# Optimization experiments

Measured on AMD Instinct MI355X. Metric: run time of the kernel, lower is better.

## Reference

```python
import jax, jax.numpy as jnp
import numpy as np

H = W = 224
N_LM = 8
BLOCK = 3  # patch is [x-3:x+3, y-3:y+3] -> 6x6


def _clip_coords(lm_float):
    # lm_float: [B, 16] normalized landmarks in [0,1]
    c = (lm_float * 224.0).astype(jnp.int32)
    c = jnp.where(c >= 219, 200, c)
    c = jnp.where(c <= 5, 8, c)
    return c.reshape(c.shape[0], N_LM, 2)


def _gather_patches(pred_map, coords):
    # pred_map: [B,1,H,W], coords: [B,8,2] int32 -> [B,8,36]
    B = pred_map.shape[0]
    x = coords[..., 0]  # [B,8]
    y = coords[..., 1]
    offs = jnp.arange(-BLOCK, BLOCK)  # 6 offsets
    xs = x[..., None] + offs          # [B,8,6]
    ys = y[..., None] + offs          # [B,8,6]
    b = jnp.arange(B)[:, None, None, None]
    # vectorized gather replacing the per-sample/per-landmark python loop
    patches = pred_map[b, 0, xs[:, :, :, None], ys[:, :, None, :]]  # [B,8,6,6]
    return patches.reshape(B, N_LM, (2 * BLOCK) ** 2)


def setup_inputs() -> dict:
    key = jax.random.key(0)
    ks = jax.random.split(key, 8)
    B = 512
    pred_map = jax.random.normal(ks[0], (B, 1, H, W), dtype=jnp.float32)
    Landmarks_GT = jax.random.uniform(ks[1], (B, 16), dtype=jnp.float32)
    d_in = H * W  # 50176
    s1 = 1.0 / np.sqrt(d_in)
    s2 = 1.0 / np.sqrt(512)
    s3 = 1.0 / np.sqrt(256)
    W1 = jax.random.uniform(ks[2], (d_in, 512), jnp.float32, -s1, s1)
    b1 = jax.random.uniform(ks[3], (512,), jnp.float32, -s1, s1)
    W2 = jax.random.uniform(ks[4], (512, 256), jnp.float32, -s2, s2)
    b2 = jax.random.uniform(ks[5], (256,), jnp.float32, -s2, s2)
    W3 = jax.random.uniform(ks[6], (256, 16), jnp.float32, -s3, s3)
    b3 = jax.random.uniform(ks[7], (16,), jnp.float32, -s3, s3)
    return {"pred_map": pred_map, "Landmarks_GT": Landmarks_GT,
            "W1": W1, "b1": b1, "W2": W2, "b2": b2, "W3": W3, "b3": b3}


def reference(pred_map, Landmarks_GT, W1, b1, W2, b2, W3, b3):
    B = pred_map.shape[0]
    # GT landmark patch gather
    gt_coords = _clip_coords(Landmarks_GT)
    GT_patch = _gather_patches(pred_map, gt_coords)  # [B,8,36]
    # MLP_Grah_Second on flattened pred_map
    flat = pred_map.reshape(B, -1)                   # [B,50176]
    h = jax.nn.relu(flat @ W1 + b1)
    h = jax.nn.relu(h @ W2 + b2)
    pred = jax.nn.sigmoid(h @ W3 + b3)               # [B,16]
    # predicted landmark patch gather
    pr_coords = _clip_coords(pred)
    Pred_patch = _gather_patches(pred_map, pr_coords)  # [B,8,36]
    return pred, GT_patch, Pred_patch
```

## Files before the change

kernel.cpp:

```cpp
#include <hip/hip_runtime.h>
#include <math.h>

typedef __fp16   h16x2 __attribute__((ext_vector_type(2)));
typedef _Float16 f16x8 __attribute__((ext_vector_type(8)));
typedef __attribute__((ext_vector_type(4))) float f32x4;

#define KDIM 50176
#define NDIM 512
#define MDIM 512
#define BM 256
#define BN 128
#define BK 32

__device__ __forceinline__ void split_pair(float a, float b, unsigned& hw, unsigned& lw) {
    h16x2 hp = __builtin_amdgcn_cvt_pkrtz(a, b);
    float ra = (a - (float)hp[0]) * 2048.0f;
    float rb = (b - (float)hp[1]) * 2048.0f;
    h16x2 lp = __builtin_amdgcn_cvt_pkrtz(ra, rb);
    union { h16x2 v; unsigned u; } cu;
    cu.v = hp; hw = cu.u;
    cu.v = lp; lw = cu.u;
}

__global__ __launch_bounds__(512, 2) void gemm1_mfma(
    const float* __restrict__ A,
    const float* __restrict__ W,
    float* __restrict__ part,
    int steps, int S)
{
    __shared__ unsigned short Ahs[2][256][40];
    __shared__ unsigned short Als[2][256][40];
    __shared__ unsigned short Bhs[2][128][40];
    __shared__ unsigned short Bls[2][128][40];

    const int t = threadIdx.x;

    const int nwg = 8 * S;
    int l = blockIdx.x;
    if ((nwg & 7) == 0) l = (l & 7) * (nwg >> 3) + (l >> 3);
    const int z = l >> 3, bm = l & 1, bn = (l >> 1) & 3;
    const int kbase = z * steps * BK;

    const int lane = t & 63, wave = t >> 6;
    const int wm = wave >> 1, wn2 = wave & 1;
    const int l15 = lane & 15, lh = lane >> 4;

    const bool isW = (t < 256);
    const int u = isW ? t : (t - 256);
    const int wkb = u & 7, wn0 = (u >> 3) * 4;
    const int achunk = u & 7, arow0 = u >> 3;

    f32x4 acc0[4][4], acc1[4][4];
#pragma unroll
    for (int i = 0; i < 4; ++i)
#pragma unroll
        for (int j = 0; j < 4; ++j) { acc0[i][j] = (f32x4)0.f; acc1[i][j] = (f32x4)0.f; }

    float4 reg[8];
    auto gload = [&](int s) {
        const int k0 = kbase + s * BK;
        if (isW) {
            const float* Wb = W + (size_t)k0 * NDIM + bn * BN + wn0;
#pragma unroll
            for (int i = 0; i < 4; ++i)
                reg[i] = *(const float4*)(Wb + (size_t)(wkb * 4 + i) * NDIM);
        } else {
            const float* Ab = A + (size_t)(bm * BM) * KDIM + k0 + achunk * 4;
#pragma unroll
            for (int j = 0; j < 8; ++j)
                reg[j] = *(const float4*)(Ab + (size_t)(arow0 + 32 * j) * KDIM);
        }
    };

    auto stageA = [&](int buf, int j) {
        unsigned h01, l01, h23, l23;
        split_pair(reg[j].x, reg[j].y, h01, l01);
        split_pair(reg[j].z, reg[j].w, h23, l23);
        *(uint2*)&Ahs[buf][arow0 + 32 * j][achunk * 4] = make_uint2(h01, h23);
        *(uint2*)&Als[buf][arow0 + 32 * j][achunk * 4] = make_uint2(l01, l23);
    };
    auto stageW = [&](int buf, int j) {
        unsigned h01, l01, h23, l23;
        split_pair(((const float*)&reg[0])[j] * 64.0f, ((const float*)&reg[1])[j] * 64.0f, h01, l01);
        split_pair(((const float*)&reg[2])[j] * 64.0f, ((const float*)&reg[3])[j] * 64.0f, h23, l23);
        *(uint2*)&Bhs[buf][wn0 + j][wkb * 4] = make_uint2(h01, h23);
        *(uint2*)&Bls[buf][wn0 + j][wkb * 4] = make_uint2(l01, l23);
    };
    auto full_stage = [&](int buf) {
        if (isW) {
#pragma unroll
            for (int j = 0; j < 4; ++j) stageW(buf, j);
        } else {
#pragma unroll
            for (int j = 0; j < 8; ++j) stageA(buf, j);
        }
    };

    gload(0);
    full_stage(0);
    __syncthreads();
    int cur = 0;
    for (int s = 0; s < steps; ++s) {
        const bool pf = (s + 1 < steps);
        if (pf) gload(s + 1);

        f16x8 ah[4], al[4];
#pragma unroll
        for (int mf = 0; mf < 4; ++mf) {
            ah[mf] = *(const f16x8*)&Ahs[cur][wm * 64 + mf * 16 + l15][lh * 8];
            al[mf] = *(const f16x8*)&Als[cur][wm * 64 + mf * 16 + l15][lh * 8];
        }
        f16x8 bh[2], bl[2];
        bh[0] = *(const f16x8*)&Bhs[cur][wn2 * 64 + l15][lh * 8];
        bl[0] = *(const f16x8*)&Bls[cur][wn2 * 64 + l15][lh * 8];

#pragma unroll
        for (int nf = 0; nf < 4; ++nf) {
            const int c = nf & 1, n = c ^ 1;
            if (nf < 3) {
                bh[n] = *(const f16x8*)&Bhs[cur][wn2 * 64 + (nf + 1) * 16 + l15][lh * 8];
                bl[n] = *(const f16x8*)&Bls[cur][wn2 * 64 + (nf + 1) * 16 + l15][lh * 8];
            }
            __builtin_amdgcn_s_setprio(1);
#pragma unroll
            for (int mf = 0; mf < 4; ++mf) {
                acc0[mf][nf] = __builtin_amdgcn_mfma_f32_16x16x32_f16(ah[mf], bh[c], acc0[mf][nf], 0, 0, 0);
                acc1[mf][nf] = __builtin_amdgcn_mfma_f32_16x16x32_f16(ah[mf], bl[c], acc1[mf][nf], 0, 0, 0);
                acc1[mf][nf] = __builtin_amdgcn_mfma_f32_16x16x32_f16(al[mf], bh[c], acc1[mf][nf], 0, 0, 0);
            }
            __builtin_amdgcn_s_setprio(0);
            if (pf) {
                if (isW) {
                    stageW(cur ^ 1, nf);
                } else {
                    stageA(cur ^ 1, 2 * nf);
                    stageA(cur ^ 1, 2 * nf + 1);
                }
            }
        }
        __syncthreads();
        cur ^= 1;
    }

    const float c0 = 1.0f / 64.0f;
    const float c1 = 1.0f / 131072.0f;
    float* Cp = part + (size_t)z * (MDIM * NDIM);
    const int row0 = bm * BM + wm * 64;
    const int col0 = bn * BN + wn2 * 64;
#pragma unroll
    for (int mf = 0; mf < 4; ++mf)
#pragma unroll
        for (int nf = 0; nf < 4; ++nf) {
            const int r0 = row0 + mf * 16 + lh * 4;
            const int c = col0 + nf * 16 + l15;
#pragma unroll
            for (int r = 0; r < 4; ++r)
                Cp[(size_t)(r0 + r) * NDIM + c] = acc0[mf][nf][r] * c0 + acc1[mf][nf][r] * c1;
        }
}

__global__ __launch_bounds__(256) void reduce_bias_relu(
    const float4* __restrict__ part, const float* __restrict__ b1,
    float4* __restrict__ h1, int S)
{
    int i = blockIdx.x * 256 + threadIdx.x;
    float4 s = make_float4(0.f, 0.f, 0.f, 0.f);
    for (int z = 0; z < S; ++z) {
        float4 v = part[(size_t)z * 65536 + i];
        s.x += v.x; s.y += v.y; s.z += v.z; s.w += v.w;
    }
    int nb = (i & 127) * 4;
    s.x = fmaxf(s.x + b1[nb + 0], 0.f);
    s.y = fmaxf(s.y + b1[nb + 1], 0.f);
    s.z = fmaxf(s.z + b1[nb + 2], 0.f);
    s.w = fmaxf(s.w + b1[nb + 3], 0.f);
    h1[i] = s;
}

__global__ __launch_bounds__(256) void gemm2_k(
    const float* __restrict__ h1, const float* __restrict__ W2,
    const float* __restrict__ b2, float* __restrict__ h2)
{
    int g = blockIdx.x * 256 + threadIdx.x;
    int m = g >> 8, n = g & 255;
    const float* a = h1 + (size_t)m * 512;
    float sum = 0.f;
#pragma unroll 8
    for (int k = 0; k < 512; ++k) sum = fmaf(a[k], W2[(size_t)k * 256 + n], sum);
    sum += b2[n];
    h2[g] = fmaxf(sum, 0.f);
}

__global__ __launch_bounds__(256) void gemm3_sig(
    const float* __restrict__ h2, const float* __restrict__ W3,
    const float* __restrict__ b3, float* __restrict__ pred)
{
    int g = blockIdx.x * 256 + threadIdx.x;
    int m = g >> 4, j = g & 15;
    const float* a = h2 + (size_t)m * 256;
    float sum = 0.f;
#pragma unroll 8
    for (int k = 0; k < 256; ++k) sum = fmaf(a[k], W3[(size_t)k * 16 + j], sum);
    sum += b3[j];
    pred[g] = 1.f / (1.f + expf(-sum));
}

__device__ __forceinline__ int clip_coord(float v) {
    int c = (int)(v * 224.0f);
    if (c >= 219) c = 200;
    if (c <= 5)   c = 8;
    return c;
}

__global__ void patches_k(
    const float* __restrict__ pm, const float* __restrict__ gt,
    const float* __restrict__ pred, float* __restrict__ out)
{
    const int b = blockIdx.x;
    const int t = threadIdx.x;
    const int lm = t / 36, cell = t % 36;
    const int dx = cell / 6 - 3, dy = cell % 6 - 3;
    const float* pmb = pm + (size_t)b * 50176;
    {
        int cx = clip_coord(gt[b * 16 + lm * 2 + 0]);
        int cy = clip_coord(gt[b * 16 + lm * 2 + 1]);
        out[8192 + b * 288 + t] = pmb[(cx + dx) * 224 + (cy + dy)];
    }
    {
        int cx = clip_coord(pred[b * 16 + lm * 2 + 0]);
        int cy = clip_coord(pred[b * 16 + lm * 2 + 1]);
        out[8192 + 147456 + b * 288 + t] = pmb[(cx + dx) * 224 + (cy + dy)];
    }
}

extern "C" void kernel_launch(void* const* d_in, const int* in_sizes, int n_in,
                              void* d_out, int out_size, void* d_ws, size_t ws_size,
                              hipStream_t stream)
{
    const float* pred_map = (const float*)d_in[0];
    const float* gt       = (const float*)d_in[1];
    const float* W1       = (const float*)d_in[2];
    const float* b1       = (const float*)d_in[3];
    const float* W2       = (const float*)d_in[4];
    const float* b2       = (const float*)d_in[5];
    const float* W3       = (const float*)d_in[6];
    const float* b3       = (const float*)d_in[7];
    float* out = (float*)d_out;

    float* h1   = (float*)d_ws;
    float* h2   = h1 + 262144;
    float* part = h2 + 131072;

    static const int cand[] = {32, 16, 8, 4, 2, 1};
    int S = 1;
    for (int i = 0; i < 6; ++i) {
        size_t need = (size_t)(393216 + (size_t)cand[i] * 262144) * sizeof(float);
        if (need <= ws_size) { S = cand[i]; break; }
    }
    const int steps = 1568 / S;

    hipLaunchKernelGGL(gemm1_mfma, dim3(8 * S), dim3(512), 0, stream,
                       pred_map, W1, part, steps, S);
    hipLaunchKernelGGL(reduce_bias_relu, dim3(256), dim3(256), 0, stream,
                       (const float4*)part, b1, (float4*)h1, S);
    hipLaunchKernelGGL(gemm2_k, dim3(131072 / 256), dim3(256), 0, stream, h1, W2, b2, h2);
    hipLaunchKernelGGL(gemm3_sig, dim3(8192 / 256), dim3(256), 0, stream, h2, W3, b3, out);
    hipLaunchKernelGGL(patches_k, dim3(512), dim3(288), 0, stream, pred_map, gt, out, out);
}
```

Measured before the change: 152.1 us.

## Load A tile directly to LDS as fp32 and split into halves at fragment read

```diff
diff --git a/kernel.cpp b/kernel.cpp
--- a/kernel.cpp
+++ b/kernel.cpp
@@ -28,8 +28,7 @@
     float* __restrict__ part,
     int steps, int S)
 {
-    __shared__ unsigned short Ahs[2][256][40];
-    __shared__ unsigned short Als[2][256][40];
+    __shared__ float          Afs[2][256][32];
     __shared__ unsigned short Bhs[2][128][40];
     __shared__ unsigned short Bls[2][128][40];
 
@@ -40,6 +39,7 @@
     if ((nwg & 7) == 0) l = (l & 7) * (nwg >> 3) + (l >> 3);
     const int z = l >> 3, bm = l & 1, bn = (l >> 1) & 3;
     const int kbase = z * steps * BK;
+    const int bmBase = bm * BM;
 
     const int lane = t & 63, wave = t >> 6;
     const int wm = wave >> 1, wn2 = wave & 1;
@@ -48,7 +48,9 @@
     const bool isW = (t < 256);
     const int u = isW ? t : (t - 256);
     const int wkb = u & 7, wn0 = (u >> 3) * 4;
-    const int achunk = u & 7, arow0 = u >> 3;
+
+    const int aRowInWave = lane >> 3;
+    const int aSwz = ((lane & 7) ^ aRowInWave) * 4;
 
     f32x4 acc0[4][4], acc1[4][4];
 #pragma unroll
@@ -56,87 +58,83 @@
 #pragma unroll
         for (int j = 0; j < 4; ++j) { acc0[i][j] = (f32x4)0.f; acc1[i][j] = (f32x4)0.f; }
 
-    float4 reg[8];
-    auto gload = [&](int s) {
+    float4 wreg[4];
+    auto gloadW = [&](int s) {
+        const float* Wb = W + (size_t)(kbase + s * BK) * NDIM + bn * BN + wn0;
+#pragma unroll
+        for (int i = 0; i < 4; ++i)
+            wreg[i] = *(const float4*)(Wb + (size_t)(wkb * 4 + i) * NDIM);
+    };
+    auto gloadA = [&](int s, int buf) {
         const int k0 = kbase + s * BK;
-        if (isW) {
-            const float* Wb = W + (size_t)k0 * NDIM + bn * BN + wn0;
-#pragma unroll
-            for (int i = 0; i < 4; ++i)
-                reg[i] = *(const float4*)(Wb + (size_t)(wkb * 4 + i) * NDIM);
-        } else {
-            const float* Ab = A + (size_t)(bm * BM) * KDIM + k0 + achunk * 4;
-#pragma unroll
-            for (int j = 0; j < 8; ++j)
-                reg[j] = *(const float4*)(Ab + (size_t)(arow0 + 32 * j) * KDIM);
-        }
-    };
-
-    auto stageA = [&](int buf, int j) {
-        unsigned h01, l01, h23, l23;
-        split_pair(reg[j].x, reg[j].y, h01, l01);
-        split_pair(reg[j].z, reg[j].w, h23, l23);
-        *(uint2*)&Ahs[buf][arow0 + 32 * j][achunk * 4] = make_uint2(h01, h23);
-        *(uint2*)&Als[buf][arow0 + 32 * j][achunk * 4] = make_uint2(l01, l23);
+#pragma unroll
+        for (int j = 0; j < 4; ++j) {
+            const int rbase = wave * 32 + j * 8;
+            const float* src = A + (size_t)(bmBase + rbase + aRowInWave) * KDIM + k0 + aSwz;
+            __builtin_amdgcn_global_load_lds(src, &Afs[buf][rbase][0], 16, 0, 0);
+        }
     };
     auto stageW = [&](int buf, int j) {
         unsigned h01, l01, h23, l23;
-        split_pair(((const float*)&reg[0])[j] * 64.0f, ((const float*)&reg[1])[j] * 64.0f, h01, l01);
-        split_pair(((const float*)&reg[2])[j] * 64.0f, ((const float*)&reg[3])[j] * 64.0f, h23, l23);
+        split_pair(((const float*)&wreg[0])[j] * 64.0f, ((const float*)&wreg[1])[j] * 64.0f, h01, l01);
+        split_pair(((const float*)&wreg[2])[j] * 64.0f, ((const float*)&wreg[3])[j] * 64.0f, h23, l23);
         *(uint2*)&Bhs[buf][wn0 + j][wkb * 4] = make_uint2(h01, h23);
         *(uint2*)&Bls[buf][wn0 + j][wkb * 4] = make_uint2(l01, l23);
     };
-    auto full_stage = [&](int buf) {
-        if (isW) {
-#pragma unroll
-            for (int j = 0; j < 4; ++j) stageW(buf, j);
-        } else {
-#pragma unroll
-            for (int j = 0; j < 8; ++j) stageA(buf, j);
-        }
-    };
-
-    gload(0);
-    full_stage(0);
+
+    auto buildA = [&](int buf, int mf, f16x8& ahv, f16x8& alv) {
+        const int m = wm * 64 + mf * 16 + l15;
+        const int s0 = ((2 * lh) ^ (l15 & 7)) * 4;
+        const int s1 = ((2 * lh + 1) ^ (l15 & 7)) * 4;
+        float4 f0 = *(const float4*)&Afs[buf][m][s0];
+        float4 f1 = *(const float4*)&Afs[buf][m][s1];
+        union { unsigned uu[4]; f16x8 v; } H, L;
+        split_pair(f0.x, f0.y, H.uu[0], L.uu[0]);
+        split_pair(f0.z, f0.w, H.uu[1], L.uu[1]);
+        split_pair(f1.x, f1.y, H.uu[2], L.uu[2]);
+        split_pair(f1.z, f1.w, H.uu[3], L.uu[3]);
+        ahv = H.v; alv = L.v;
+    };
+
+    if (isW) gloadW(0);
+    gloadA(0, 0);
+    if (isW) {
+#pragma unroll
+        for (int j = 0; j < 4; ++j) stageW(0, j);
+    }
     __syncthreads();
+
     int cur = 0;
     for (int s = 0; s < steps; ++s) {
         const bool pf = (s + 1 < steps);
-        if (pf) gload(s + 1);
-
-        f16x8 ah[4], al[4];
+        if (pf) {
+            if (isW) gloadW(s + 1);
+            gloadA(s + 1, cur ^ 1);
+        }
+
+        f16x8 bh[4], bl[4];
+#pragma unroll
+        for (int nf = 0; nf < 4; ++nf) {
+            bh[nf] = *(const f16x8*)&Bhs[cur][wn2 * 64 + nf * 16 + l15][lh * 8];
+            bl[nf] = *(const f16x8*)&Bls[cur][wn2 * 64 + nf * 16 + l15][lh * 8];
+        }
+
+        f16x8 ah[2], al[2];
+        buildA(cur, 0, ah[0], al[0]);
+
 #pragma unroll
         for (int mf = 0; mf < 4; ++mf) {
-            ah[mf] = *(const f16x8*)&Ahs[cur][wm * 64 + mf * 16 + l15][lh * 8];
-            al[mf] = *(const f16x8*)&Als[cur][wm * 64 + mf * 16 + l15][lh * 8];
-        }
-        f16x8 bh[2], bl[2];
-        bh[0] = *(const f16x8*)&Bhs[cur][wn2 * 64 + l15][lh * 8];
-        bl[0] = *(const f16x8*)&Bls[cur][wn2 * 64 + l15][lh * 8];
-
-#pragma unroll
-        for (int nf = 0; nf < 4; ++nf) {
-            const int c = nf & 1, n = c ^ 1;
-            if (nf < 3) {
-                bh[n] = *(const f16x8*)&Bhs[cur][wn2 * 64 + (nf + 1) * 16 + l15][lh * 8];
-                bl[n] = *(const f16x8*)&Bls[cur][wn2 * 64 + (nf + 1) * 16 + l15][lh * 8];
-            }
+            const int c = mf & 1, n = c ^ 1;
+            if (mf < 3) buildA(cur, mf + 1, ah[n], al[n]);
             __builtin_amdgcn_s_setprio(1);
 #pragma unroll
-            for (int mf = 0; mf < 4; ++mf) {
-                acc0[mf][nf] = __builtin_amdgcn_mfma_f32_16x16x32_f16(ah[mf], bh[c], acc0[mf][nf], 0, 0, 0);
-                acc1[mf][nf] = __builtin_amdgcn_mfma_f32_16x16x32_f16(ah[mf], bl[c], acc1[mf][nf], 0, 0, 0);
-                acc1[mf][nf] = __builtin_amdgcn_mfma_f32_16x16x32_f16(al[mf], bh[c], acc1[mf][nf], 0, 0, 0);
+            for (int nf = 0; nf < 4; ++nf) {
+                acc0[mf][nf] = __builtin_amdgcn_mfma_f32_16x16x32_f16(ah[c], bh[nf], acc0[mf][nf], 0, 0, 0);
+                acc1[mf][nf] = __builtin_amdgcn_mfma_f32_16x16x32_f16(ah[c], bl[nf], acc1[mf][nf], 0, 0, 0);
+                acc1[mf][nf] = __builtin_amdgcn_mfma_f32_16x16x32_f16(al[c], bh[nf], acc1[mf][nf], 0, 0, 0);
             }
             __builtin_amdgcn_s_setprio(0);
-            if (pf) {
-                if (isW) {
-                    stageW(cur ^ 1, nf);
-                } else {
-                    stageA(cur ^ 1, 2 * nf);
-                    stageA(cur ^ 1, 2 * nf + 1);
-                }
-            }
+            if (pf && isW) stageW(cur ^ 1, mf);
         }
         __syncthreads();
         cur ^= 1;
@@ -145,7 +143,7 @@
     const float c0 = 1.0f / 64.0f;
     const float c1 = 1.0f / 131072.0f;
     float* Cp = part + (size_t)z * (MDIM * NDIM);
-    const int row0 = bm * BM + wm * 64;
+    const int row0 = bmBase + wm * 64;
     const int col0 = bn * BN + wn2 * 64;
 #pragma unroll
     for (int mf = 0; mf < 4; ++mf)
```

Result: slower. 159.0 us (+4.5%).

## Halve GEMM1 M-tile, double workgroups, and swizzle merged A hi/lo LDS layout

Applied to the files above, without the earlier changes.

```diff
diff --git a/kernel.cpp b/kernel.cpp
--- a/kernel.cpp
+++ b/kernel.cpp
@@ -8,9 +8,10 @@
 #define KDIM 50176
 #define NDIM 512
 #define MDIM 512
-#define BM 256
+#define BM 128
 #define BN 128
 #define BK 32
+#define NSTEPS 1568
 
 __device__ __forceinline__ void split_pair(float a, float b, unsigned& hw, unsigned& lw) {
     h16x2 hp = __builtin_amdgcn_cvt_pkrtz(a, b);
@@ -22,41 +23,41 @@
     cu.v = lp; lw = cu.u;
 }
 
-__global__ __launch_bounds__(512, 2) void gemm1_mfma(
+__global__ __launch_bounds__(512, 4) void gemm1_mfma_v3(
     const float* __restrict__ A,
     const float* __restrict__ W,
     float* __restrict__ part,
     int steps, int S)
 {
-    __shared__ unsigned short Ahs[2][256][40];
-    __shared__ unsigned short Als[2][256][40];
+    __shared__ unsigned short Apls[2][128 * 64];
     __shared__ unsigned short Bhs[2][128][40];
     __shared__ unsigned short Bls[2][128][40];
 
     const int t = threadIdx.x;
 
-    const int nwg = 8 * S;
+    const int nwg = 16 * S;
     int l = blockIdx.x;
     if ((nwg & 7) == 0) l = (l & 7) * (nwg >> 3) + (l >> 3);
-    const int z = l >> 3, bm = l & 1, bn = (l >> 1) & 3;
+    const int z = l >> 4, bm = l & 3, bn = (l >> 2) & 3;
     const int kbase = z * steps * BK;
+    const int bmBase = bm * BM;
 
     const int lane = t & 63, wave = t >> 6;
-    const int wm = wave >> 1, wn2 = wave & 1;
+    const int wm = wave >> 2, wn = wave & 3;
     const int l15 = lane & 15, lh = lane >> 4;
 
     const bool isW = (t < 256);
     const int u = isW ? t : (t - 256);
     const int wkb = u & 7, wn0 = (u >> 3) * 4;
-    const int achunk = u & 7, arow0 = u >> 3;
-
-    f32x4 acc0[4][4], acc1[4][4];
+    const int arow = u >> 3, akq = u & 7;
+
+    f32x4 acc0[4][2], acc1[4][2];
 #pragma unroll
     for (int i = 0; i < 4; ++i)
 #pragma unroll
-        for (int j = 0; j < 4; ++j) { acc0[i][j] = (f32x4)0.f; acc1[i][j] = (f32x4)0.f; }
-
-    float4 reg[8];
+        for (int j = 0; j < 2; ++j) { acc0[i][j] = (f32x4)0.f; acc1[i][j] = (f32x4)0.f; }
+
+    float4 reg[4];
     auto gload = [&](int s) {
         const int k0 = kbase + s * BK;
         if (isW) {
@@ -65,20 +66,13 @@
             for (int i = 0; i < 4; ++i)
                 reg[i] = *(const float4*)(Wb + (size_t)(wkb * 4 + i) * NDIM);
         } else {
-            const float* Ab = A + (size_t)(bm * BM) * KDIM + k0 + achunk * 4;
-#pragma unroll
-            for (int j = 0; j < 8; ++j)
-                reg[j] = *(const float4*)(Ab + (size_t)(arow0 + 32 * j) * KDIM);
-        }
-    };
-
-    auto stageA = [&](int buf, int j) {
-        unsigned h01, l01, h23, l23;
-        split_pair(reg[j].x, reg[j].y, h01, l01);
-        split_pair(reg[j].z, reg[j].w, h23, l23);
-        *(uint2*)&Ahs[buf][arow0 + 32 * j][achunk * 4] = make_uint2(h01, h23);
-        *(uint2*)&Als[buf][arow0 + 32 * j][achunk * 4] = make_uint2(l01, l23);
-    };
+            const float* Ab = A + (size_t)(bmBase + arow) * KDIM + k0 + akq * 4;
+#pragma unroll
+            for (int j = 0; j < 4; ++j)
+                reg[j] = *(const float4*)(Ab + (size_t)(32 * j) * KDIM);
+        }
+    };
+
     auto stageW = [&](int buf, int j) {
         unsigned h01, l01, h23, l23;
         split_pair(((const float*)&reg[0])[j] * 64.0f, ((const float*)&reg[1])[j] * 64.0f, h01, l01);
@@ -86,57 +80,60 @@
         *(uint2*)&Bhs[buf][wn0 + j][wkb * 4] = make_uint2(h01, h23);
         *(uint2*)&Bls[buf][wn0 + j][wkb * 4] = make_uint2(l01, l23);
     };
+    auto stageA = [&](int buf, int j) {
+        const int r = arow + 32 * j;
+        unsigned h0, h1, l0, l1;
+        split_pair(reg[j].x, reg[j].y, h0, l0);
+        split_pair(reg[j].z, reg[j].w, h1, l1);
+        const int kg = akq >> 1, hs = akq & 1;
+        unsigned short* base = &Apls[buf][r * 64];
+        *(uint2*)(base + ((kg ^ (r & 7)) * 8 + hs * 4))       = make_uint2(h0, h1);
+        *(uint2*)(base + (((4 | kg) ^ (r & 7)) * 8 + hs * 4)) = make_uint2(l0, l1);
+    };
     auto full_stage = [&](int buf) {
-        if (isW) {
-#pragma unroll
-            for (int j = 0; j < 4; ++j) stageW(buf, j);
-        } else {
-#pragma unroll
-            for (int j = 0; j < 8; ++j) stageA(buf, j);
-        }
+#pragma unroll
+        for (int j = 0; j < 4; ++j) { if (isW) stageW(buf, j); else stageA(buf, j); }
     };
 
     gload(0);
     full_stage(0);
     __syncthreads();
+
     int cur = 0;
     for (int s = 0; s < steps; ++s) {
         const bool pf = (s + 1 < steps);
         if (pf) gload(s + 1);
 
-        f16x8 ah[4], al[4];
+        f16x8 bh[2], bl[2];
+#pragma unroll
+        for (int nf = 0; nf < 2; ++nf) {
+            bh[nf] = *(const f16x8*)&Bhs[cur][wn * 32 + nf * 16 + l15][lh * 8];
+            bl[nf] = *(const f16x8*)&Bls[cur][wn * 32 + nf * 16 + l15][lh * 8];
+        }
+
+        f16x8 ah[2], al[2];
+        {
+            const int m = wm * 64 + l15;
+            ah[0] = *(const f16x8*)&Apls[cur][m * 64 + ((lh ^ (m & 7)) * 8)];
+            al[0] = *(const f16x8*)&Apls[cur][m * 64 + (((4 | lh) ^ (m & 7)) * 8)];
+        }
 #pragma unroll
         for (int mf = 0; mf < 4; ++mf) {
-            ah[mf] = *(const f16x8*)&Ahs[cur][wm * 64 + mf * 16 + l15][lh * 8];
-            al[mf] = *(const f16x8*)&Als[cur][wm * 64 + mf * 16 + l15][lh * 8];
-        }
-        f16x8 bh[2], bl[2];
-        bh[0] = *(const f16x8*)&Bhs[cur][wn2 * 64 + l15][lh * 8];
-        bl[0] = *(const f16x8*)&Bls[cur][wn2 * 64 + l15][lh * 8];
-
-#pragma unroll
-        for (int nf = 0; nf < 4; ++nf) {
-            const int c = nf & 1, n = c ^ 1;
-            if (nf < 3) {
-                bh[n] = *(const f16x8*)&Bhs[cur][wn2 * 64 + (nf + 1) * 16 + l15][lh * 8];
-                bl[n] = *(const f16x8*)&Bls[cur][wn2 * 64 + (nf + 1) * 16 + l15][lh * 8];
+            const int c = mf & 1, n = c ^ 1;
+            if (mf < 3) {
+                const int m = wm * 64 + (mf + 1) * 16 + l15;
+                ah[n] = *(const f16x8*)&Apls[cur][m * 64 + ((lh ^ (m & 7)) * 8)];
+                al[n] = *(const f16x8*)&Apls[cur][m * 64 + (((4 | lh) ^ (m & 7)) * 8)];
             }
             __builtin_amdgcn_s_setprio(1);
 #pragma unroll
-            for (int mf = 0; mf < 4; ++mf) {
-                acc0[mf][nf] = __builtin_amdgcn_mfma_f32_16x16x32_f16(ah[mf], bh[c], acc0[mf][nf], 0, 0, 0);
-                acc1[mf][nf] = __builtin_amdgcn_mfma_f32_16x16x32_f16(ah[mf], bl[c], acc1[mf][nf], 0, 0, 0);
-                acc1[mf][nf] = __builtin_amdgcn_mfma_f32_16x16x32_f16(al[mf], bh[c], acc1[mf][nf], 0, 0, 0);
+            for (int nf = 0; nf < 2; ++nf) {
+                acc0[mf][nf] = __builtin_amdgcn_mfma_f32_16x16x32_f16(ah[c], bh[nf], acc0[mf][nf], 0, 0, 0);
+                acc1[mf][nf] = __builtin_amdgcn_mfma_f32_16x16x32_f16(ah[c], bl[nf], acc1[mf][nf], 0, 0, 0);
+                acc1[mf][nf] = __builtin_amdgcn_mfma_f32_16x16x32_f16(al[c], bh[nf], acc1[mf][nf], 0, 0, 0);
             }
             __builtin_amdgcn_s_setprio(0);
-            if (pf) {
-                if (isW) {
-                    stageW(cur ^ 1, nf);
-                } else {
-                    stageA(cur ^ 1, 2 * nf);
-                    stageA(cur ^ 1, 2 * nf + 1);
-                }
-            }
+            if (pf) { if (isW) stageW(cur ^ 1, mf); else stageA(cur ^ 1, mf); }
         }
         __syncthreads();
         cur ^= 1;
@@ -145,12 +142,12 @@
     const float c0 = 1.0f / 64.0f;
     const float c1 = 1.0f / 131072.0f;
     float* Cp = part + (size_t)z * (MDIM * NDIM);
-    const int row0 = bm * BM + wm * 64;
-    const int col0 = bn * BN + wn2 * 64;
+    const int row0 = bmBase + wm * 64;
+    const int col0 = bn * BN + wn * 32;
 #pragma unroll
     for (int mf = 0; mf < 4; ++mf)
 #pragma unroll
-        for (int nf = 0; nf < 4; ++nf) {
+        for (int nf = 0; nf < 2; ++nf) {
             const int r0 = row0 + mf * 16 + lh * 4;
             const int c = col0 + nf * 16 + l15;
 #pragma unroll
@@ -257,9 +254,9 @@
         size_t need = (size_t)(393216 + (size_t)cand[i] * 262144) * sizeof(float);
         if (need <= ws_size) { S = cand[i]; break; }
     }
-    const int steps = 1568 / S;
-
-    hipLaunchKernelGGL(gemm1_mfma, dim3(8 * S), dim3(512), 0, stream,
+    const int steps = NSTEPS / S;
+
+    hipLaunchKernelGGL(gemm1_mfma_v3, dim3(16 * S), dim3(512), 0, stream,
                        pred_map, W1, part, steps, S);
     hipLaunchKernelGGL(reduce_bias_relu, dim3(256), dim3(256), 0, stream,
                        (const float4*)part, b1, (float4*)h1, S);
```

New measurement: 205.4 us. +35.0%, slower.

## Split fp16 hi/lo product terms across separate workgroups to cut LDS and registers

Applied to the files above, without the earlier changes.

```diff
diff --git a/kernel.cpp b/kernel.cpp
--- a/kernel.cpp
+++ b/kernel.cpp
@@ -11,35 +11,38 @@
 #define BM 256
 #define BN 128
 #define BK 32
-
-__device__ __forceinline__ void split_pair(float a, float b, unsigned& hw, unsigned& lw) {
+#define NSTEPS 1568
+
+__device__ __forceinline__ unsigned pk_h(float a, float b) {
+    union { h16x2 v; unsigned u; } cu;
+    cu.v = __builtin_amdgcn_cvt_pkrtz(a, b);
+    return cu.u;
+}
+__device__ __forceinline__ unsigned pk_l(float a, float b) {
     h16x2 hp = __builtin_amdgcn_cvt_pkrtz(a, b);
     float ra = (a - (float)hp[0]) * 2048.0f;
     float rb = (b - (float)hp[1]) * 2048.0f;
-    h16x2 lp = __builtin_amdgcn_cvt_pkrtz(ra, rb);
-    union { h16x2 v; unsigned u; } cu;
-    cu.v = hp; hw = cu.u;
-    cu.v = lp; lw = cu.u;
-}
-
-__global__ __launch_bounds__(512, 2) void gemm1_mfma(
+    return pk_h(ra, rb);
+}
+
+__global__ __launch_bounds__(512, 4) void gemm1_mfma_v5(
     const float* __restrict__ A,
     const float* __restrict__ W,
     float* __restrict__ part,
     int steps, int S)
 {
-    __shared__ unsigned short Ahs[2][256][40];
-    __shared__ unsigned short Als[2][256][40];
-    __shared__ unsigned short Bhs[2][128][40];
-    __shared__ unsigned short Bls[2][128][40];
+    __shared__ unsigned short Ai[2][256][40];
+    __shared__ unsigned short Bi[2][128][40];
 
     const int t = threadIdx.x;
 
-    const int nwg = 8 * S;
+    const int nwg = 24 * S;
     int l = blockIdx.x;
     if ((nwg & 7) == 0) l = (l & 7) * (nwg >> 3) + (l >> 3);
-    const int z = l >> 3, bm = l & 1, bn = (l >> 1) & 3;
-    const int kbase = z * steps * BK;
+    const int bm = l & 1, bn = (l >> 1) & 3, zf = l >> 3;
+    const int ks = zf / 3, p = zf - ks * 3;
+    const int kbase = ks * steps * BK;
+    const int bmBase = bm * BM, bnBase = bn * BN;
 
     const int lane = t & 63, wave = t >> 6;
     const int wm = wave >> 1, wn2 = wave & 1;
@@ -50,91 +53,92 @@
     const int wkb = u & 7, wn0 = (u >> 3) * 4;
     const int achunk = u & 7, arow0 = u >> 3;
 
-    f32x4 acc0[4][4], acc1[4][4];
+    f32x4 acc[4][4];
 #pragma unroll
     for (int i = 0; i < 4; ++i)
 #pragma unroll
-        for (int j = 0; j < 4; ++j) { acc0[i][j] = (f32x4)0.f; acc1[i][j] = (f32x4)0.f; }
-
-    float4 reg[8];
-    auto gload = [&](int s) {
-        const int k0 = kbase + s * BK;
-        if (isW) {
-            const float* Wb = W + (size_t)k0 * NDIM + bn * BN + wn0;
-#pragma unroll
-            for (int i = 0; i < 4; ++i)
-                reg[i] = *(const float4*)(Wb + (size_t)(wkb * 4 + i) * NDIM);
-        } else {
-            const float* Ab = A + (size_t)(bm * BM) * KDIM + k0 + achunk * 4;
-#pragma unroll
-            for (int j = 0; j < 8; ++j)
-                reg[j] = *(const float4*)(Ab + (size_t)(arow0 + 32 * j) * KDIM);
-        }
-    };
-
-    auto stageA = [&](int buf, int j) {
-        unsigned h01, l01, h23, l23;
-        split_pair(reg[j].x, reg[j].y, h01, l01);
-        split_pair(reg[j].z, reg[j].w, h23, l23);
-        *(uint2*)&Ahs[buf][arow0 + 32 * j][achunk * 4] = make_uint2(h01, h23);
-        *(uint2*)&Als[buf][arow0 + 32 * j][achunk * 4] = make_uint2(l01, l23);
-    };
+        for (int j = 0; j < 4; ++j) acc[i][j] = (f32x4)0.f;
+
+    float4 reg[4];
+    auto gloadW = [&](int s) {
+        const float* Wb = W + (size_t)(kbase + s * BK) * NDIM + bnBase + wn0;
+#pragma unroll
+        for (int i = 0; i < 4; ++i)
+            reg[i] = *(const float4*)(Wb + (size_t)(wkb * 4 + i) * NDIM);
+    };
+    auto gloadA_half = [&](int s, int half) {
+        const float* Ab = A + (size_t)(bmBase + arow0 + half * 128) * KDIM
+                            + kbase + s * BK + achunk * 4;
+#pragma unroll
+        for (int j = 0; j < 4; ++j)
+            reg[j] = *(const float4*)(Ab + (size_t)(32 * j) * KDIM);
+    };
+
     auto stageW = [&](int buf, int j) {
-        unsigned h01, l01, h23, l23;
-        split_pair(((const float*)&reg[0])[j] * 64.0f, ((const float*)&reg[1])[j] * 64.0f, h01, l01);
-        split_pair(((const float*)&reg[2])[j] * 64.0f, ((const float*)&reg[3])[j] * 64.0f, h23, l23);
-        *(uint2*)&Bhs[buf][wn0 + j][wkb * 4] = make_uint2(h01, h23);
-        *(uint2*)&Bls[buf][wn0 + j][wkb * 4] = make_uint2(l01, l23);
-    };
-    auto full_stage = [&](int buf) {
-        if (isW) {
-#pragma unroll
-            for (int j = 0; j < 4; ++j) stageW(buf, j);
-        } else {
-#pragma unroll
-            for (int j = 0; j < 8; ++j) stageA(buf, j);
-        }
-    };
-
-    gload(0);
-    full_stage(0);
+        float v0 = ((const float*)&reg[0])[j] * 64.0f;
+        float v1 = ((const float*)&reg[1])[j] * 64.0f;
+        float v2 = ((const float*)&reg[2])[j] * 64.0f;
+        float v3 = ((const float*)&reg[3])[j] * 64.0f;
+        unsigned w01, w23;
+        if (p == 1) { w01 = pk_l(v0, v1); w23 = pk_l(v2, v3); }
+        else        { w01 = pk_h(v0, v1); w23 = pk_h(v2, v3); }
+        *(uint2*)&Bi[buf][wn0 + j][wkb * 4] = make_uint2(w01, w23);
+    };
+    auto stageA = [&](int buf, int half, int j) {
+        float4 f = reg[j];
+        unsigned w01, w23;
+        if (p == 2) { w01 = pk_l(f.x, f.y); w23 = pk_l(f.z, f.w); }
+        else        { w01 = pk_h(f.x, f.y); w23 = pk_h(f.z, f.w); }
+        *(uint2*)&Ai[buf][arow0 + half * 128 + 32 * j][achunk * 4] = make_uint2(w01, w23);
+    };
+
+    if (isW) {
+        gloadW(0);
+#pragma unroll
+        for (int j = 0; j < 4; ++j) stageW(0, j);
+    } else {
+        gloadA_half(0, 0);
+#pragma unroll
+        for (int j = 0; j < 4; ++j) stageA(0, 0, j);
+        gloadA_half(0, 1);
+#pragma unroll
+        for (int j = 0; j < 4; ++j) stageA(0, 1, j);
+    }
     __syncthreads();
+
     int cur = 0;
     for (int s = 0; s < steps; ++s) {
         const bool pf = (s + 1 < steps);
-        if (pf) gload(s + 1);
-
-        f16x8 ah[4], al[4];
-#pragma unroll
-        for (int mf = 0; mf < 4; ++mf) {
-            ah[mf] = *(const f16x8*)&Ahs[cur][wm * 64 + mf * 16 + l15][lh * 8];
-            al[mf] = *(const f16x8*)&Als[cur][wm * 64 + mf * 16 + l15][lh * 8];
+        if (pf) {
+            if (isW) gloadW(s + 1);
+            else     gloadA_half(s + 1, 0);
         }
-        f16x8 bh[2], bl[2];
-        bh[0] = *(const f16x8*)&Bhs[cur][wn2 * 64 + l15][lh * 8];
-        bl[0] = *(const f16x8*)&Bls[cur][wn2 * 64 + l15][lh * 8];
+
+        f16x8 af[4];
+#pragma unroll
+        for (int mf = 0; mf < 4; ++mf)
+            af[mf] = *(const f16x8*)&Ai[cur][wm * 64 + mf * 16 + l15][lh * 8];
+        f16x8 bf[2];
+        bf[0] = *(const f16x8*)&Bi[cur][wn2 * 64 + l15][lh * 8];
 
 #pragma unroll
         for (int nf = 0; nf < 4; ++nf) {
             const int c = nf & 1, n = c ^ 1;
-            if (nf < 3) {
-                bh[n] = *(const f16x8*)&Bhs[cur][wn2 * 64 + (nf + 1) * 16 + l15][lh * 8];
-                bl[n] = *(const f16x8*)&Bls[cur][wn2 * 64 + (nf + 1) * 16 + l15][lh * 8];
-            }
+            if (nf < 3)
+                bf[n] = *(const f16x8*)&Bi[cur][wn2 * 64 + (nf + 1) * 16 + l15][lh * 8];
             __builtin_amdgcn_s_setprio(1);
 #pragma unroll
-            for (int mf = 0; mf < 4; ++mf) {
-                acc0[mf][nf] = __builtin_amdgcn_mfma_f32_16x16x32_f16(ah[mf], bh[c], acc0[mf][nf], 0, 0, 0);
-                acc1[mf][nf] = __builtin_amdgcn_mfma_f32_16x16x32_f16(ah[mf], bl[c], acc1[mf][nf], 0, 0, 0);
-                acc1[mf][nf] = __builtin_amdgcn_mfma_f32_16x16x32_f16(al[mf], bh[c], acc1[mf][nf], 0, 0, 0);
-            }
+            for (int mf = 0; mf < 4; ++mf)
+                acc[mf][nf] = __builtin_amdgcn_mfma_f32_16x16x32_f16(af[mf], bf[c], acc[mf][nf], 0, 0, 0);
             __builtin_amdgcn_s_setprio(0);
             if (pf) {
                 if (isW) {
                     stageW(cur ^ 1, nf);
                 } else {
-                    stageA(cur ^ 1, 2 * nf);
-                    stageA(cur ^ 1, 2 * nf + 1);
+                    const int half = nf >> 1, j0 = (nf & 1) * 2;
+                    stageA(cur ^ 1, half, j0);
+                    stageA(cur ^ 1, half, j0 + 1);
+                    if (nf == 1) gloadA_half(s + 1, 1);
                 }
             }
         }
@@ -142,11 +146,10 @@
         cur ^= 1;
     }
 
-    const float c0 = 1.0f / 64.0f;
-    const float c1 = 1.0f / 131072.0f;
-    float* Cp = part + (size_t)z * (MDIM * NDIM);
-    const int row0 = bm * BM + wm * 64;
-    const int col0 = bn * BN + wn2 * 64;
+    const float scale = (p == 0) ? (1.0f / 64.0f) : (1.0f / 131072.0f);
+    float* Cp = part + (size_t)zf * (MDIM * NDIM);
+    const int row0 = bmBase + wm * 64;
+    const int col0 = bnBase + wn2 * 64;
 #pragma unroll
     for (int mf = 0; mf < 4; ++mf)
 #pragma unroll
@@ -155,17 +158,17 @@
             const int c = col0 + nf * 16 + l15;
 #pragma unroll
             for (int r = 0; r < 4; ++r)
-                Cp[(size_t)(r0 + r) * NDIM + c] = acc0[mf][nf][r] * c0 + acc1[mf][nf][r] * c1;
+                Cp[(size_t)(r0 + r) * NDIM + c] = acc[mf][nf][r] * scale;
         }
 }
 
 __global__ __launch_bounds__(256) void reduce_bias_relu(
     const float4* __restrict__ part, const float* __restrict__ b1,
-    float4* __restrict__ h1, int S)
+    float4* __restrict__ h1, int zsl)
 {
     int i = blockIdx.x * 256 + threadIdx.x;
     float4 s = make_float4(0.f, 0.f, 0.f, 0.f);
-    for (int z = 0; z < S; ++z) {
+    for (int z = 0; z < zsl; ++z) {
         float4 v = part[(size_t)z * 65536 + i];
         s.x += v.x; s.y += v.y; s.z += v.z; s.w += v.w;
     }
@@ -254,15 +257,16 @@
     static const int cand[] = {32, 16, 8, 4, 2, 1};
     int S = 1;
     for (int i = 0; i < 6; ++i) {
-        size_t need = (size_t)(393216 + (size_t)cand[i] * 262144) * sizeof(float);
+        size_t need = (size_t)(393216 + (size_t)(3 * cand[i]) * 262144) * sizeof(float);
         if (need <= ws_size) { S = cand[i]; break; }
     }
-    const int steps = 1568 / S;
-
-    hipLaunchKernelGGL(gemm1_mfma, dim3(8 * S), dim3(512), 0, stream,
+    const int steps = NSTEPS / S;
+    const int zsl = 3 * S;
+
+    hipLaunchKernelGGL(gemm1_mfma_v5, dim3(8 * zsl), dim3(512), 0, stream,
                        pred_map, W1, part, steps, S);
     hipLaunchKernelGGL(reduce_bias_relu, dim3(256), dim3(256), 0, stream,
-                       (const float4*)part, b1, (float4*)h1, S);
+                       (const float4*)part, b1, (float4*)h1, zsl);
     hipLaunchKernelGGL(gemm2_k, dim3(131072 / 256), dim3(256), 0, stream, h1, W2, b2, h2);
     hipLaunchKernelGGL(gemm3_sig, dim3(8192 / 256), dim3(256), 0, stream, h2, W3, b3, out);
     hipLaunchKernelGGL(patches_k, dim3(512), dim3(288), 0, stream, pred_map, gt, out, out);
```

After: 286.4 us. 88.4% more time.
